# Performance work log

Hardware: AMD Instinct MI355X
Metric: run time of the kernel (lower is better)

## Reference

```python
import jax, jax.numpy as jnp
import numpy as np

B, D_MODEL, H, W = 4, 128, 128, 128
HEAD_DIM = 16
GROUP = D_MODEL // HEAD_DIM          # 8 deformable groups
D_INNER = D_MODEL                    # expand = 1
D_STATE = 1
DT_RANK = 8                          # ceil(d_model / 16)
D_CONV = 3
EPS = 1e-6


def setup_inputs() -> dict:
    key = jax.random.key(0)
    ks = jax.random.split(key, 10)
    f = jnp.float32
    # dt bias init as in DASSM.dt_init (dt in [1e-3, 1e-1], inverse-softplus)
    dt = jnp.exp(jax.random.uniform(ks[7], (D_INNER,), f)
                 * (np.log(0.1) - np.log(0.001)) + np.log(0.001))
    dt = jnp.clip(dt, 1e-4)
    dt_b = dt + jnp.log(-jnp.expm1(-dt))
    s = DT_RANK ** -0.5
    return dict(
        x=jax.random.normal(ks[0], (B, D_MODEL, H, W), f),
        in_proj_w=jax.random.normal(ks[1], (D_INNER, D_MODEL), f) * (D_MODEL ** -0.5),
        conv2d_w=jax.random.normal(ks[2], (D_INNER, 1, D_CONV, D_CONV), f) * 0.1,
        conv2d_b=jnp.zeros((D_INNER,), f),
        dw_w=jax.random.normal(ks[3], (D_INNER, 1, 3, 3), f) * 0.1,
        dw_b=jnp.zeros((D_INNER,), f),
        dw_ln_g=jnp.ones((D_INNER,), f),
        dw_ln_b=jnp.zeros((D_INNER,), f),
        off_w=jax.random.normal(ks[4], (GROUP * 2, D_INNER), f) * 0.01,
        off_b=jnp.zeros((GROUP * 2,), f),
        x_proj_w=jax.random.normal(ks[5], (DT_RANK + 2 * D_STATE, D_INNER), f) * (D_INNER ** -0.5),
        dt_w=jax.random.uniform(ks[6], (D_INNER, DT_RANK), f, -s, s),
        dt_b=dt_b,
        A_logs=jnp.tile(jnp.log(jnp.arange(1, D_STATE + 1, dtype=f))[None, :], (D_INNER, 1)),
        Ds=jnp.ones((D_INNER,), f),
        out_ln_g=jnp.ones((D_INNER,), f),
        out_ln_b=jnp.zeros((D_INNER,), f),
        out_proj_w=jax.random.normal(ks[8], (D_MODEL, D_INNER), f) * (D_INNER ** -0.5),
    )


def _layer_norm(x, g, b):
    m = x.mean(-1, keepdims=True)
    v = ((x - m) ** 2).mean(-1, keepdims=True)
    return (x - m) * jax.lax.rsqrt(v + EPS) * g + b


def _dwconv(x, w, b):
    # x: (B,C,H,W), w: (C,1,k,k) depthwise, 'SAME' == torch padding=(k-1)//2
    out = jax.lax.conv_general_dilated(
        x, w, (1, 1), 'SAME', feature_group_count=x.shape[1],
        dimension_numbers=('NCHW', 'OIHW', 'NCHW'))
    return out + b[None, :, None, None]


def _dcn_sample(img_last, offset):
    # DCNv3 with kernel_size=1, mask=1: sampling point = pixel center + offset.
    # img_last: (B,H,W,C); offset: (B,H,W,G*2) laid out (x,y) per group.
    b, h, w, c = img_last.shape
    gc = c // GROUP
    img = img_last.reshape(b, h, w, GROUP, gc)
    off = offset.reshape(b, h, w, GROUP, 2)
    px = jnp.arange(w, dtype=offset.dtype)[None, None, :, None] + off[..., 0]
    py = jnp.arange(h, dtype=offset.dtype)[None, :, None, None] + off[..., 1]
    y0 = jnp.floor(py)
    x0 = jnp.floor(px)
    wy = py - y0
    wx = px - x0
    bi = jnp.arange(b)[:, None, None, None]
    gi = jnp.arange(GROUP)[None, None, None, :]

    def tap(yi, xi, wgt):  # zero-padding bilinear tap (grid_sample, align_corners=False)
        valid = (yi >= 0) & (yi < h) & (xi >= 0) & (xi < w)
        yc = jnp.clip(yi, 0, h - 1).astype(jnp.int32)
        xc = jnp.clip(xi, 0, w - 1).astype(jnp.int32)
        v = img[bi, yc, xc, gi]  # (B,H,W,G,gc)
        return v * (wgt * valid)[..., None]

    out = (tap(y0, x0, (1 - wy) * (1 - wx)) + tap(y0, x0 + 1, (1 - wy) * wx)
           + tap(y0 + 1, x0, wy * (1 - wx)) + tap(y0 + 1, x0 + 1, wy * wx))
    return out.reshape(b, h, w, c)


def _selective_scan(xs, dts, A, Bs, Cs, Ds, dt_bias):
    # xs,dts: (B,D,L); A: (D,N); Bs,Cs: (B,N,L); delta_softplus=True
    delta = jax.nn.softplus(dts + dt_bias[None, :, None])
    dA = jnp.exp(jnp.einsum('bdl,dn->lbdn', delta, A))          # (L,B,D,N)
    dBx = jnp.einsum('bdl,bnl,bdl->lbdn', delta, Bs, xs)          # (L,B,D,N)
    C_t = jnp.transpose(Cs, (2, 0, 1))                            # (L,B,N)

    def step(hc, inputs):
        dA_t, dBx_t, c = inputs
        hc = dA_t * hc + dBx_t
        return hc, jnp.einsum('bdn,bn->bd', hc, c)

    h0 = jnp.zeros(dA.shape[1:], xs.dtype)
    _, ys = jax.lax.scan(step, h0, (dA, dBx, C_t))                # ys: (L,B,D)
    y = jnp.transpose(ys, (1, 2, 0))                              # (B,D,L)
    return y + Ds[None, :, None] * xs


def reference(x, in_proj_w, conv2d_w, conv2d_b, dw_w, dw_b, dw_ln_g, dw_ln_b,
              off_w, off_b, x_proj_w, dt_w, dt_b, A_logs, Ds,
              out_ln_g, out_ln_b, out_proj_w):
    # in_proj (1x1 conv, no bias) then depthwise conv + SiLU
    xin = jnp.einsum('bchw,oc->bohw', x, in_proj_w)
    xc = jax.nn.silu(_dwconv(xin, conv2d_w, conv2d_b))
    # Dynamic_Adaptive_Scan: dwconv -> LN(channels_last) -> GELU -> offsets -> DCNv3(k=1)
    x1 = _dwconv(xc, dw_w, dw_b)
    x1 = jax.nn.gelu(_layer_norm(jnp.transpose(x1, (0, 2, 3, 1)), dw_ln_g, dw_ln_b),
                     approximate=False)
    offset = x1 @ off_w.T + off_b                                  # (B,H,W,G*2)
    xd = _dcn_sample(jnp.transpose(xc, (0, 2, 3, 1)), offset)      # (B,H,W,C)
    xd = jnp.transpose(xd, (0, 3, 1, 2))                           # (B,C,H,W)
    # SSM (Mamba selective scan over L = H*W)
    Bn, C, Hh, Ww = xd.shape
    L = Hh * Ww
    xs = xd.reshape(Bn, C, L)
    x_dbl = jnp.einsum('rc,bcl->brl', x_proj_w, xs)
    dts, Bs, Cs = jnp.split(x_dbl, [DT_RANK, DT_RANK + D_STATE], axis=1)
    dts = jnp.einsum('dr,brl->bdl', dt_w, dts)
    A = -jnp.exp(A_logs)
    y = _selective_scan(xs, dts, A, Bs, Cs, Ds, dt_b).reshape(Bn, C, Hh, Ww)
    # out LayerNorm (over channels) + out_proj (1x1, no bias)
    y = jnp.transpose(_layer_norm(jnp.transpose(y, (0, 2, 3, 1)), out_ln_g, out_ln_b),
                      (0, 3, 1, 2))
    return jnp.einsum('bchw,oc->bohw', y, out_proj_w)
```

## Files before the change

### kernel.cpp

```cpp
#include <hip/hip_runtime.h>
#include <hip/hip_bf16.h>

typedef unsigned short u16;
typedef unsigned int u32;
typedef __bf16 bf16x8 __attribute__((ext_vector_type(8)));
typedef float f32x4 __attribute__((ext_vector_type(4)));

__device__ __forceinline__ float bfu(u16 u) { return __uint_as_float(((u32)u) << 16); }
__device__ __forceinline__ u16 fbf(float f) {
  __hip_bfloat16 h = __float2bfloat16(f);
  return *reinterpret_cast<u16*>(&h);
}
__device__ __forceinline__ float softplusf(float z) {
  float t = __expf(z);
  return (z > 20.f) ? z : __logf(1.f + t);
}
__device__ __forceinline__ float lo16(u32 p) { return __uint_as_float(p << 16); }
__device__ __forceinline__ float hi16(u32 p) { return __uint_as_float(p & 0xffff0000u); }
__device__ __forceinline__ bf16x8 ld_bf8(const u16* p) {
  union { uint4 u; bf16x8 v; } c;
  c.u = *(const uint4*)p;
  return c.v;
}


__global__ __launch_bounds__(256) void k_inproj(const float* __restrict__ X,
                                                const float* __restrict__ W,
                                                u16* __restrict__ out,
                                                const float* __restrict__ W2,
                                                const float* __restrict__ gO,
                                                const float* __restrict__ bO,
                                                float* __restrict__ s12) {
  __shared__ __align__(16) u16 Ws[128 * 136];
  __shared__ __align__(16) u16 Xs[64 * 136];
  int tid = threadIdx.x;
  if (blockIdx.x == 1024) {
    if (tid < 128) {
      int o = tid;
      float s1 = 0.f, s2 = 0.f;
      for (int c = 0; c < 128; ++c) {
        float w = W2[(o << 7) + c];
        s1 = fmaf(w, bO[c], s1);
        s2 = fmaf(w, gO[c], s2);
      }
      s12[o] = s1;
      s12[128 + o] = s2;
    }
    return;
  }
  int b = blockIdx.x >> 8;
  int l0 = (blockIdx.x & 255) << 6;
  for (int i = 0; i < 16; ++i) {
    int idx = (i << 8) + tid;
    int o = idx >> 5, c4 = (idx & 31) << 2;
    float4 w4 = *(const float4*)&W[(o << 7) + c4];
    ushort4 s;
    s.x = fbf(w4.x); s.y = fbf(w4.y); s.z = fbf(w4.z); s.w = fbf(w4.w);
    *(ushort4*)&Ws[o * 136 + c4] = s;
  }
  for (int i = 0; i < 8; ++i) {
    int idx = (i << 8) + tid;
    int c = idx >> 4, lq = (idx & 15) << 2;
    float4 x4 = *(const float4*)&X[(((long)(b << 7) + c) << 14) + l0 + lq];
    Xs[(lq + 0) * 136 + c] = fbf(x4.x);
    Xs[(lq + 1) * 136 + c] = fbf(x4.y);
    Xs[(lq + 2) * 136 + c] = fbf(x4.z);
    Xs[(lq + 3) * 136 + c] = fbf(x4.w);
  }
  __syncthreads();
  int w = tid >> 6, lane = tid & 63;
  int mrow = lane & 15, quad = lane >> 4;
  f32x4 acc[2][4];
#pragma unroll
  for (int ot = 0; ot < 2; ++ot)
#pragma unroll
    for (int lt = 0; lt < 4; ++lt) acc[ot][lt] = (f32x4){0.f, 0.f, 0.f, 0.f};
#pragma unroll
  for (int kb = 0; kb < 4; ++kb) {
    int c0 = (kb << 5) + (quad << 3);
    bf16x8 af[2], bfr[4];
#pragma unroll
    for (int ot = 0; ot < 2; ++ot)
      af[ot] = ld_bf8(&Ws[((w << 5) + (ot << 4) + mrow) * 136 + c0]);
#pragma unroll
    for (int lt = 0; lt < 4; ++lt)
      bfr[lt] = ld_bf8(&Xs[((lt << 4) + mrow) * 136 + c0]);
#pragma unroll
    for (int ot = 0; ot < 2; ++ot)
#pragma unroll
      for (int lt = 0; lt < 4; ++lt)
        acc[ot][lt] = __builtin_amdgcn_mfma_f32_16x16x32_bf16(af[ot], bfr[lt], acc[ot][lt], 0, 0, 0);
  }
#pragma unroll
  for (int ot = 0; ot < 2; ++ot)
#pragma unroll
    for (int lt = 0; lt < 4; ++lt) {
      int l = l0 + (lt << 4) + mrow;
      int o = (w << 5) + (ot << 4) + (quad << 2);
      ushort4 s;
      s.x = fbf(acc[ot][lt][0]); s.y = fbf(acc[ot][lt][1]);
      s.z = fbf(acc[ot][lt][2]); s.w = fbf(acc[ot][lt][3]);
      *(ushort4*)&out[(((long)(b << 14) + l) << 7) + o] = s;
    }
}

__global__ __launch_bounds__(256) void k_dwconv(const u16* __restrict__ in,
                                                const float* __restrict__ w9,
                                                const float* __restrict__ bias,
                                                u16* __restrict__ out) {
  __shared__ float wsT[9][128];
  __shared__ float bs[128];
  int tid = threadIdx.x;
  for (int i = 0; i < 5; ++i) {
    int lin = (i << 8) + tid;
    if (lin < 1152) { int c = lin / 9, k = lin - 9 * c; wsT[k][c] = w9[lin]; }
  }
  if (tid < 128) bs[tid] = bias[tid];
  __syncthreads();
  int blk = blockIdx.x;
  int b = blk >> 10;
  int s = blk & 1023;
  int h = s >> 3;
  int w = ((s & 7) << 4) + (tid >> 4);
  int c0 = (tid & 15) << 3;
  const u16* bbase = in + ((long)b << 21);
  float acc[8];
  {
    float4 b0 = *(const float4*)&bs[c0];
    float4 b1 = *(const float4*)&bs[c0 + 4];
    acc[0] = b0.x; acc[1] = b0.y; acc[2] = b0.z; acc[3] = b0.w;
    acc[4] = b1.x; acc[5] = b1.y; acc[6] = b1.z; acc[7] = b1.w;
  }
#pragma unroll
  for (int ky = -1; ky <= 1; ++ky) {
    int y = h + ky;
    if ((unsigned)y >= 128u) continue;
#pragma unroll
    for (int kx = -1; kx <= 1; ++kx) {
      int x = w + kx;
      if ((unsigned)x >= 128u) continue;
      int k = (ky + 1) * 3 + (kx + 1);
      uint4 v = *(const uint4*)(bbase + ((((y << 7) + x)) << 7) + c0);
      float4 w0 = *(const float4*)&wsT[k][c0];
      float4 w1 = *(const float4*)&wsT[k][c0 + 4];
      u32 vv[4] = {v.x, v.y, v.z, v.w};
      float wf[8] = {w0.x, w0.y, w0.z, w0.w, w1.x, w1.y, w1.z, w1.w};
#pragma unroll
      for (int cc = 0; cc < 8; ++cc) {
        float xv = (cc & 1) ? hi16(vv[cc >> 1]) : lo16(vv[cc >> 1]);
        acc[cc] = fmaf(wf[cc], xv, acc[cc]);
      }
    }
  }
#pragma unroll
  for (int cc = 0; cc < 8; ++cc) acc[cc] = acc[cc] / (1.f + __expf(-acc[cc]));
  int g4 = c0 >> 4, sub = c0 & 15;
  uint4 pkst;
  pkst.x = (u32)fbf(acc[0]) | ((u32)fbf(acc[1]) << 16);
  pkst.y = (u32)fbf(acc[2]) | ((u32)fbf(acc[3]) << 16);
  pkst.z = (u32)fbf(acc[4]) | ((u32)fbf(acc[5]) << 16);
  pkst.w = (u32)fbf(acc[6]) | ((u32)fbf(acc[7]) << 16);
  u16* po = out + (((long)(b << 3) + g4) << 18) + ((((h << 7) + w)) << 4) + sub;
  *(uint4*)po = pkst;
}

__global__ __launch_bounds__(256) void k_dwoff(const u16* __restrict__ in,
                                               const float* __restrict__ w9,
                                               const float* __restrict__ bias,
                                               const float* __restrict__ g,
                                               const float* __restrict__ bt,
                                               const float* __restrict__ offw,
                                               const float* __restrict__ offb,
                                               float* __restrict__ offs) {
  __shared__ float wsT[9][128];
  __shared__ float bs[128], gs[128], bsh[128];
  __shared__ __align__(16) u16 Ge[16 * 136];
  __shared__ __align__(16) u16 Wos[16 * 136];
  int tid = threadIdx.x;
  for (int i = 0; i < 5; ++i) {
    int lin = (i << 8) + tid;
    if (lin < 1152) { int c = lin / 9, k = lin - 9 * c; wsT[k][c] = w9[lin]; }
  }
  if (tid < 128) { bs[tid] = bias[tid]; gs[tid] = g[tid]; bsh[tid] = bt[tid]; }
  for (int i = 0; i < 8; ++i) {
    int idx = (i << 8) + tid;
    int o = idx >> 7, c = idx & 127;
    Wos[o * 136 + c] = fbf(offw[idx]);
  }
  __syncthreads();
  int blk = blockIdx.x;
  int b = blk >> 10;
  int s = blk & 1023;
  int h = s >> 3;
  int p = tid >> 4;
  int w = ((s & 7) << 4) + p;
  int c0 = (tid & 15) << 3;
  int g4 = c0 >> 4, sub = c0 & 15;
  const u16* bbase = in + (((long)(b << 3) + g4) << 18) + sub;
  float acc[8];
  {
    float4 b0 = *(const float4*)&bs[c0];
    float4 b1 = *(const float4*)&bs[c0 + 4];
    acc[0] = b0.x; acc[1] = b0.y; acc[2] = b0.z; acc[3] = b0.w;
    acc[4] = b1.x; acc[5] = b1.y; acc[6] = b1.z; acc[7] = b1.w;
  }
#pragma unroll
  for (int ky = -1; ky <= 1; ++ky) {
    int y = h + ky;
    if ((unsigned)y >= 128u) continue;
#pragma unroll
    for (int kx = -1; kx <= 1; ++kx) {
      int x = w + kx;
      if ((unsigned)x >= 128u) continue;
      int k = (ky + 1) * 3 + (kx + 1);
      uint4 v = *(const uint4*)(bbase + ((((y << 7) + x)) << 4));
      float4 w0 = *(const float4*)&wsT[k][c0];
      float4 w1 = *(const float4*)&wsT[k][c0 + 4];
      u32 vv[4] = {v.x, v.y, v.z, v.w};
      float wf[8] = {w0.x, w0.y, w0.z, w0.w, w1.x, w1.y, w1.z, w1.w};
#pragma unroll
      for (int cc = 0; cc < 8; ++cc) {
        float xv = (cc & 1) ? hi16(vv[cc >> 1]) : lo16(vv[cc >> 1]);
        acc[cc] = fmaf(wf[cc], xv, acc[cc]);
      }
    }
  }
  float sum = 0.f, ssum = 0.f;
#pragma unroll
  for (int cc = 0; cc < 8; ++cc) { sum += acc[cc]; ssum = fmaf(acc[cc], acc[cc], ssum); }
#pragma unroll
  for (int off = 1; off < 16; off <<= 1) {
    sum += __shfl_xor(sum, off);
    ssum += __shfl_xor(ssum, off);
  }
  float m = sum * (1.f / 128.f);
  float r = rsqrtf(ssum * (1.f / 128.f) - m * m + 1e-6f);
  {
    u32 pk[4];
#pragma unroll
    for (int jj = 0; jj < 4; ++jj) {
      u16 h2[2];
#pragma unroll
      for (int e = 0; e < 2; ++e) {
        int cc = 2 * jj + e;
        float xn = fmaf((acc[cc] - m) * r, gs[c0 + cc], bsh[c0 + cc]);
        h2[e] = fbf(0.5f * xn * (1.f + erff(xn * 0.70710678118f)));
      }
      pk[jj] = (u32)h2[0] | ((u32)h2[1] << 16);
    }
    *(uint4*)&Ge[p * 136 + c0] = make_uint4(pk[0], pk[1], pk[2], pk[3]);
  }
  __syncthreads();
  if (tid < 64) {
    int lane = tid;
    int mrow = lane & 15, quad = lane >> 4;
    f32x4 acc0 = (f32x4){0.f, 0.f, 0.f, 0.f};
#pragma unroll
    for (int kb = 0; kb < 4; ++kb) {
      int cb = (kb << 5) + (quad << 3);
      bf16x8 af = ld_bf8(&Wos[mrow * 136 + cb]);
      bf16x8 bfr = ld_bf8(&Ge[mrow * 136 + cb]);
      acc0 = __builtin_amdgcn_mfma_f32_16x16x32_bf16(af, bfr, acc0, 0, 0, 0);
    }
    int l = (h << 7) + ((s & 7) << 4) + mrow;
    float2* po = (float2*)offs;
    int o0 = quad << 2;
    po[(((long)((b << 3) + (quad << 1))) << 14) + l] =
        make_float2(acc0[0] + offb[o0], acc0[1] + offb[o0 + 1]);
    po[(((long)((b << 3) + (quad << 1) + 1)) << 14) + l] =
        make_float2(acc0[2] + offb[o0 + 2], acc0[3] + offb[o0 + 3]);
  }
}

__global__ __launch_bounds__(512, 8) void k_dcn(const u16* __restrict__ xc,
                                                const float* __restrict__ offs,
                                                const float* __restrict__ xpw,
                                                const float* __restrict__ dtw,
                                                u16* __restrict__ xs,
                                                u16* __restrict__ dts,
                                                float* __restrict__ Bsb,
                                                float* __restrict__ Csb) {
  __shared__ __align__(16) u16 xds_bf[64 * 132];
  __shared__ float part[64 * 81];
  __shared__ __align__(16) float xdblT[8 * 64];
  int tid = threadIdx.x;
  int blk = blockIdx.x;
  int b = blk >> 8;
  int l0 = (blk & 255) << 6;
  int p = tid & 63, gg = tid >> 6;
  int l = l0 + p, hh = l >> 7, ww = l & 127;
  float2 off = ((const float2*)offs)[(((long)((b << 3) + gg)) << 14) + l];
  float px = (float)ww + off.x, py = (float)hh + off.y;
  float x0f = floorf(px), y0f = floorf(py);
  float wx = px - x0f, wy = py - y0f;
  int ix = (int)x0f, iy = (int)y0f;
  int x0c = min(max(ix, 0), 127), x1c = min(max(ix + 1, 0), 127);
  int y0c = min(max(iy, 0), 127), y1c = min(max(iy + 1, 0), 127);
  float vx0 = ((unsigned)ix < 128u) ? 1.f : 0.f;
  float vx1 = ((unsigned)(ix + 1) < 128u) ? 1.f : 0.f;
  float vy0 = ((unsigned)iy < 128u) ? 1.f : 0.f;
  float vy1 = ((unsigned)(iy + 1) < 128u) ? 1.f : 0.f;
  float wt4[4] = {(1.f - wy) * (1.f - wx) * vy0 * vx0,
                  (1.f - wy) * wx * vy0 * vx1,
                  wy * (1.f - wx) * vy1 * vx0,
                  wy * wx * vy1 * vx1};
  const u16* bbase = xc + (((long)(b << 3) + gg) << 18);
  const u16* r0p = bbase + ((((y0c << 7) + x0c)) << 4);
  const u16* r1p = bbase + ((((y1c << 7) + x0c)) << 4);
  uint4 q0 = ((const uint4*)r0p)[0];
  uint4 q1 = ((const uint4*)r0p)[1];
  uint4 q2 = ((const uint4*)r0p)[2];
  uint4 q3 = ((const uint4*)r0p)[3];
  uint4 q4 = ((const uint4*)r1p)[0];
  uint4 q5 = ((const uint4*)r1p)[1];
  uint4 q6 = ((const uint4*)r1p)[2];
  uint4 q7 = ((const uint4*)r1p)[3];
  bool adj = (x1c != x0c);
  u32 t0[8] = {q0.x, q0.y, q0.z, q0.w, q1.x, q1.y, q1.z, q1.w};
  u32 t1[8] = {adj ? q2.x : q0.x, adj ? q2.y : q0.y, adj ? q2.z : q0.z, adj ? q2.w : q0.w,
               adj ? q3.x : q1.x, adj ? q3.y : q1.y, adj ? q3.z : q1.z, adj ? q3.w : q1.w};
  u32 t2[8] = {q4.x, q4.y, q4.z, q4.w, q5.x, q5.y, q5.z, q5.w};
  u32 t3[8] = {adj ? q6.x : q4.x, adj ? q6.y : q4.y, adj ? q6.z : q4.z, adj ? q6.w : q4.w,
               adj ? q7.x : q5.x, adj ? q7.y : q5.y, adj ? q7.z : q5.z, adj ? q7.w : q5.w};
  float acc[16];
#pragma unroll
  for (int ch = 0; ch < 16; ++ch) acc[ch] = 0.f;
#pragma unroll
  for (int ch = 0; ch < 16; ++ch) {
    float v0 = (ch & 1) ? hi16(t0[ch >> 1]) : lo16(t0[ch >> 1]);
    float v1 = (ch & 1) ? hi16(t1[ch >> 1]) : lo16(t1[ch >> 1]);
    float v2 = (ch & 1) ? hi16(t2[ch >> 1]) : lo16(t2[ch >> 1]);
    float v3 = (ch & 1) ? hi16(t3[ch >> 1]) : lo16(t3[ch >> 1]);
    float a = fmaf(wt4[0], v0, wt4[1] * v1);
    a = fmaf(wt4[2], v2, a);
    acc[ch] = fmaf(wt4[3], v3, a);
  }
  {
    u32 pk[8];
#pragma unroll
    for (int j = 0; j < 8; ++j)
      pk[j] = (u32)fbf(acc[2 * j]) | ((u32)fbf(acc[2 * j + 1]) << 16);
    u16* row = &xds_bf[p * 132 + (gg << 4)];
#pragma unroll
    for (int q = 0; q < 4; ++q)
      *(uint2*)(row + (q << 2)) = make_uint2(pk[2 * q], pk[2 * q + 1]);
  }
  {
    int ggu = __builtin_amdgcn_readfirstlane(gg);
    const float* wb = xpw + (ggu << 4);
    int pbase = p * 81 + gg;
#pragma unroll
    for (int r = 0; r < 10; ++r) {
      const float* wr = wb + (r << 7);
      float s = 0.f;
#pragma unroll
      for (int ch = 0; ch < 16; ++ch) s = fmaf(wr[ch], acc[ch], s);
      part[pbase + (r << 3)] = s;
    }
  }
  __syncthreads();
  {
    int task = tid;
#pragma unroll
    for (int pass = 0; pass < 2; ++pass, task += 512) {
      if (task < 640) {
        int r = task >> 6, p2 = task & 63;
        const float* pp = &part[p2 * 81 + (r << 3)];
        float s = ((pp[0] + pp[1]) + (pp[2] + pp[3])) + ((pp[4] + pp[5]) + (pp[6] + pp[7]));
        if (r < 8) xdblT[(r << 6) + p2] = s;
        else if (r == 8) Bsb[((long)b << 14) + l0 + p2] = s;
        else Csb[((long)b << 14) + l0 + p2] = s;
      }
    }
  }
#pragma unroll
  for (int it = 0; it < 2; ++it) {
    int task = (it << 9) + tid;
    int cc = task >> 3, t = task & 7;
    u32 pk[4];
#pragma unroll
    for (int jj = 0; jj < 4; ++jj) {
      u16 a0 = xds_bf[((t << 3) + 2 * jj + 0) * 132 + cc];
      u16 a1 = xds_bf[((t << 3) + 2 * jj + 1) * 132 + cc];
      pk[jj] = (u32)a0 | ((u32)a1 << 16);
    }
    *(uint4*)&xs[(((long)(b << 7) + cc) << 14) + l0 + (t << 3)] =
        make_uint4(pk[0], pk[1], pk[2], pk[3]);
  }
  __syncthreads();
  {
    int dd = tid >> 3, t = tid & 7;
    float4 a0 = *(const float4*)&dtw[dd << 3];
    float4 a1 = *(const float4*)&dtw[(dd << 3) + 4];
    float4 b0 = *(const float4*)&dtw[(dd + 64) << 3];
    float4 b1 = *(const float4*)&dtw[((dd + 64) << 3) + 4];
    float wr0[8] = {a0.x, a0.y, a0.z, a0.w, a1.x, a1.y, a1.z, a1.w};
    float wr1[8] = {b0.x, b0.y, b0.z, b0.w, b1.x, b1.y, b1.z, b1.w};
    float y0[8], y1[8];
#pragma unroll
    for (int j = 0; j < 8; ++j) { y0[j] = 0.f; y1[j] = 0.f; }
#pragma unroll
    for (int rr = 0; rr < 8; ++rr) {
      float w0 = wr0[rr], w1 = wr1[rr];
      const float* xr = &xdblT[(rr << 6) + (t << 3)];
      float4 xa = *(const float4*)xr;
      float4 xb = *(const float4*)(xr + 4);
      float xv[8] = {xa.x, xa.y, xa.z, xa.w, xb.x, xb.y, xb.z, xb.w};
#pragma unroll
      for (int j = 0; j < 8; ++j) {
        y0[j] = fmaf(w0, xv[j], y0[j]);
        y1[j] = fmaf(w1, xv[j], y1[j]);
      }
    }
    u32 pk0[4], pk1[4];
#pragma unroll
    for (int jj = 0; jj < 4; ++jj) {
      pk0[jj] = (u32)fbf(y0[2 * jj]) | ((u32)fbf(y0[2 * jj + 1]) << 16);
      pk1[jj] = (u32)fbf(y1[2 * jj]) | ((u32)fbf(y1[2 * jj + 1]) << 16);
    }
    *(uint4*)&dts[(((long)(b << 7) + dd) << 14) + l0 + (t << 3)] =
        make_uint4(pk0[0], pk0[1], pk0[2], pk0[3]);
    *(uint4*)&dts[(((long)(b << 7) + dd + 64) << 14) + l0 + (t << 3)] =
        make_uint4(pk1[0], pk1[1], pk1[2], pk1[3]);
  }
}

__global__ __launch_bounds__(1024) void k_scan(u16* __restrict__ xy,
                                               const u16* __restrict__ dts16,
                                               const float* __restrict__ Bsb,
                                               const float* __restrict__ Csb,
                                               const float* __restrict__ A_logs,
                                               const float* __restrict__ Dsv,
                                               const float* __restrict__ dtbv) {
  __shared__ float swp[16], swe[16];
  int bd = blockIdx.x;
  int b = bd >> 7, d = bd & 127;
  float Ad = -__expf(A_logs[d]);
  float dtb = dtbv[d];
  float Dd = Dsv[d];
  int t = threadIdx.x;
  int lane = t & 63, wid = t >> 6;
  long base = ((long)bd << 14) + (t << 4);
  long bb = ((long)b << 14) + (t << 4);
  const uint4* pz4 = (const uint4*)(dts16 + base);
  const uint4* px4 = (const uint4*)(xy + base);
  const float4* pB = (const float4*)(Bsb + bb);
  const float4* pC = (const float4*)(Csb + bb);
  uint4 zA = pz4[0], zB = pz4[1];
  uint4 xA = px4[0], xB = px4[1];
  u32 zw[8] = {zA.x, zA.y, zA.z, zA.w, zB.x, zB.y, zB.z, zB.w};
  u32 xw[8] = {xA.x, xA.y, xA.z, xA.w, xB.x, xB.y, xB.z, xB.w};
  float E = 0.f, P = 1.f;
#pragma unroll
  for (int q = 0; q < 4; ++q) {
    float4 B4 = pB[q];
    float Bq[4] = {B4.x, B4.y, B4.z, B4.w};
#pragma unroll
    for (int j = 0; j < 4; ++j) {
      int k = (q << 2) + j;
      float z = (k & 1) ? hi16(zw[k >> 1]) : lo16(zw[k >> 1]);
      float xv = (k & 1) ? hi16(xw[k >> 1]) : lo16(xw[k >> 1]);
      float delta = softplusf(z + dtb);
      float a = __expf(delta * Ad);
      E = fmaf(a, E, delta * Bq[j] * xv);
      P *= a;
    }
  }
#pragma unroll
  for (int off = 1; off < 64; off <<= 1) {
    float Pp = __shfl_up(P, off);
    float Ep = __shfl_up(E, off);
    if (lane >= off) { E = fmaf(P, Ep, E); P *= Pp; }
  }
  if (lane == 63) { swp[wid] = P; swe[wid] = E; }
  __syncthreads();
  if (t < 16) {
    float p2 = swp[t], e2 = swe[t];
#pragma unroll
    for (int off = 1; off < 16; off <<= 1) {
      float pp = __shfl_up(p2, off);
      float ee = __shfl_up(e2, off);
      if (t >= off) { e2 = fmaf(p2, ee, e2); p2 *= pp; }
    }
    swp[t] = p2; swe[t] = e2;
  }
  __syncthreads();
  float hw = (wid == 0) ? 0.f : swe[wid - 1];
  float Pex = __shfl_up(P, 1);
  float Eex = __shfl_up(E, 1);
  if (lane == 0) { Pex = 1.f; Eex = 0.f; }
  float h = fmaf(Pex, hw, Eex);
  u32 ypk[8];
#pragma unroll
  for (int q = 0; q < 4; ++q) {
    float4 B4 = pB[q];
    float4 C4 = pC[q];
    float Bq[4] = {B4.x, B4.y, B4.z, B4.w};
    float Cq[4] = {C4.x, C4.y, C4.z, C4.w};
#pragma unroll
    for (int j = 0; j < 4; ++j) {
      int k = (q << 2) + j;
      float z = (k & 1) ? hi16(zw[k >> 1]) : lo16(zw[k >> 1]);
      float xv = (k & 1) ? hi16(xw[k >> 1]) : lo16(xw[k >> 1]);
      float delta = softplusf(z + dtb);
      float a = __expf(delta * Ad);
      h = fmaf(a, h, delta * Bq[j] * xv);
      u16 yb = fbf(fmaf(Dd, xv, h * Cq[j]));
      if ((k & 1) == 0) ypk[k >> 1] = yb; else ypk[k >> 1] |= (u32)yb << 16;
    }
  }
  uint4* py = (uint4*)(xy + base);
  py[0] = make_uint4(ypk[0], ypk[1], ypk[2], ypk[3]);
  py[1] = make_uint4(ypk[4], ypk[5], ypk[6], ypk[7]);
}

__global__ __launch_bounds__(256) void k_outproj(const u16* __restrict__ y,
                                                 const float* __restrict__ W2,
                                                 const float* __restrict__ g,
                                                 const float* __restrict__ s12,
                                                 float* __restrict__ out) {
  __shared__ __align__(16) u16 Ws[128 * 136];
  __shared__ __align__(16) u16 Ys[64 * 136];
  __shared__ float ps[4][64], pss[4][64];
  __shared__ float mean_s[64], rstd_s[64];
  int tid = threadIdx.x;
  int b = blockIdx.x >> 8;
  int l0 = (blockIdx.x & 255) << 6;
  for (int i = 0; i < 16; ++i) {
    int idx = (i << 8) + tid;
    int o = idx >> 5, c4 = (idx & 31) << 2;
    float4 w4 = *(const float4*)&W2[(o << 7) + c4];
    ushort4 s;
    s.x = fbf(w4.x * g[c4]);     s.y = fbf(w4.y * g[c4 + 1]);
    s.z = fbf(w4.z * g[c4 + 2]); s.w = fbf(w4.w * g[c4 + 3]);
    *(ushort4*)&Ws[o * 136 + c4] = s;
  }
  for (int i = 0; i < 4; ++i) {
    int idx = (i << 8) + tid;
    int c = idx >> 3, lq = (idx & 7) << 3;
    uint4 v = *(const uint4*)&y[(((long)(b << 7) + c) << 14) + l0 + lq];
    u32 vv[4] = {v.x, v.y, v.z, v.w};
#pragma unroll
    for (int r = 0; r < 8; ++r)
      Ys[(lq + r) * 136 + c] = (u16)((r & 1) ? (vv[r >> 1] >> 16) : (vv[r >> 1] & 0xffffu));
  }
  __syncthreads();
  {
    int l = tid & 63, q = tid >> 6;
    const u16* row = &Ys[l * 136 + (q << 5)];
    float s = 0.f, ss = 0.f;
#pragma unroll 8
    for (int c = 0; c < 32; ++c) { float v = bfu(row[c]); s += v; ss = fmaf(v, v, ss); }
    ps[q][l] = s; pss[q][l] = ss;
  }
  __syncthreads();
  if (tid < 64) {
    float s = ps[0][tid] + ps[1][tid] + ps[2][tid] + ps[3][tid];
    float ss = pss[0][tid] + pss[1][tid] + pss[2][tid] + pss[3][tid];
    float m = s * (1.f / 128.f);
    mean_s[tid] = m;
    rstd_s[tid] = rsqrtf(ss * (1.f / 128.f) - m * m + 1e-6f);
  }
  __syncthreads();
  int w = tid >> 6, lane = tid & 63;
  int mrow = lane & 15, quad = lane >> 4;
  f32x4 acc[2][4];
#pragma unroll
  for (int ot = 0; ot < 2; ++ot)
#pragma unroll
    for (int lt = 0; lt < 4; ++lt) acc[ot][lt] = (f32x4){0.f, 0.f, 0.f, 0.f};
#pragma unroll
  for (int kb = 0; kb < 4; ++kb) {
    int c0 = (kb << 5) + (quad << 3);
    bf16x8 af[2], bfr[4];
#pragma unroll
    for (int ot = 0; ot < 2; ++ot)
      af[ot] = ld_bf8(&Ws[((w << 5) + (ot << 4) + mrow) * 136 + c0]);
#pragma unroll
    for (int lt = 0; lt < 4; ++lt)
      bfr[lt] = ld_bf8(&Ys[((lt << 4) + mrow) * 136 + c0]);
#pragma unroll
    for (int ot = 0; ot < 2; ++ot)
#pragma unroll
      for (int lt = 0; lt < 4; ++lt)
        acc[ot][lt] = __builtin_amdgcn_mfma_f32_16x16x32_bf16(af[ot], bfr[lt], acc[ot][lt], 0, 0, 0);
  }
  float s1r[2][4], s2r[2][4];
#pragma unroll
  for (int ot = 0; ot < 2; ++ot)
#pragma unroll
    for (int r = 0; r < 4; ++r) {
      int o = (w << 5) + (ot << 4) + (quad << 2) + r;
      s1r[ot][r] = s12[o];
      s2r[ot][r] = s12[128 + o];
    }
#pragma unroll
  for (int ot = 0; ot < 2; ++ot)
#pragma unroll
    for (int lt = 0; lt < 4; ++lt) {
      int lcol = (lt << 4) + mrow;
      float mv = mean_s[lcol], rv = rstd_s[lcol];
      int obase = (w << 5) + (ot << 4) + (quad << 2);
#pragma unroll
      for (int r = 0; r < 4; ++r) {
        float v = fmaf(rv, acc[ot][lt][r] - mv * s2r[ot][r], s1r[ot][r]);
        out[(((long)(b << 7) + obase + r) << 14) + l0 + lcol] = v;
      }
    }
}

extern "C" void kernel_launch(void* const* d_in, const int* in_sizes, int n_in,
                              void* d_out, int out_size, void* d_ws, size_t ws_size,
                              hipStream_t stream) {
  const float* x         = (const float*)d_in[0];
  const float* in_proj_w = (const float*)d_in[1];
  const float* conv2d_w  = (const float*)d_in[2];
  const float* conv2d_b  = (const float*)d_in[3];
  const float* dw_w      = (const float*)d_in[4];
  const float* dw_b      = (const float*)d_in[5];
  const float* dw_ln_g   = (const float*)d_in[6];
  const float* dw_ln_b   = (const float*)d_in[7];
  const float* off_w     = (const float*)d_in[8];
  const float* off_b     = (const float*)d_in[9];
  const float* x_proj_w  = (const float*)d_in[10];
  const float* dt_w      = (const float*)d_in[11];
  const float* dt_b      = (const float*)d_in[12];
  const float* A_logs    = (const float*)d_in[13];
  const float* Ds        = (const float*)d_in[14];
  const float* out_ln_g  = (const float*)d_in[15];
  const float* out_ln_b  = (const float*)d_in[16];
  const float* out_proj_w= (const float*)d_in[17];
  float* out = (float*)d_out;

  u16* A  = (u16*)d_ws;
  u16* Bx = A + 8388608;
  u16* Dd = Bx + 8388608;
  float* offs  = (float*)(Dd + 8388608);
  float* Bsb   = offs + 1048576;
  float* Csb   = Bsb + 65536;
  float* s12   = Csb + 65536;

  hipLaunchKernelGGL(k_inproj, dim3(1025), dim3(256), 0, stream, x, in_proj_w, A,
                     out_proj_w, out_ln_g, out_ln_b, s12);
  hipLaunchKernelGGL(k_dwconv, dim3(4096), dim3(256), 0, stream, A, conv2d_w, conv2d_b, Bx);
  hipLaunchKernelGGL(k_dwoff, dim3(4096), dim3(256), 0, stream, Bx, dw_w, dw_b,
                     dw_ln_g, dw_ln_b, off_w, off_b, offs);
  hipLaunchKernelGGL(k_dcn, dim3(1024), dim3(512), 0, stream, Bx, offs, x_proj_w, dt_w, A, Dd, Bsb, Csb);
  hipLaunchKernelGGL(k_scan, dim3(512), dim3(1024), 0, stream, A, Dd, Bsb, Csb, A_logs, Ds, dt_b);
  hipLaunchKernelGGL(k_outproj, dim3(1024), dim3(256), 0, stream, A, out_proj_w, out_ln_g, s12, out);
}
```

Measured before the change: 218.8 us.

## Fuse offset-generation kernel into deformable sampling kernel via shared memory

Merges the depthwise conv + LayerNorm + GELU + offset-projection kernel into the DCN sampling kernel, so each 64-pixel block computes its own offsets into shared memory instead of writing them to global memory and reading them back. This removes one launch and the global round-trip of the offset buffer. Shared memory is aliased across phases through a union buffer, and launch bounds drop from 8 to 6 blocks per SM. Each thread now handles 16 channels of the dwconv with per-element weight loads from LDS, which may raise register pressure and lower occupancy.

Measured after the change: 209.5 us. 4.3% less time.

```diff
diff --git a/kernel.cpp b/kernel.cpp
--- a/kernel.cpp
+++ b/kernel.cpp
@@ -164,132 +164,120 @@
   *(uint4*)po = pkst;
 }
 
-__global__ __launch_bounds__(256) void k_dwoff(const u16* __restrict__ in,
-                                               const float* __restrict__ w9,
-                                               const float* __restrict__ bias,
-                                               const float* __restrict__ g,
-                                               const float* __restrict__ bt,
-                                               const float* __restrict__ offw,
-                                               const float* __restrict__ offb,
-                                               float* __restrict__ offs) {
-  __shared__ float wsT[9][128];
+__global__ __launch_bounds__(512, 6) void k_dcnoff(const u16* __restrict__ xc,
+                                                   const float* __restrict__ w9,
+                                                   const float* __restrict__ bias,
+                                                   const float* __restrict__ g,
+                                                   const float* __restrict__ bt,
+                                                   const float* __restrict__ offw,
+                                                   const float* __restrict__ offb,
+                                                   const float* __restrict__ xpw,
+                                                   const float* __restrict__ dtw,
+                                                   u16* __restrict__ xs,
+                                                   u16* __restrict__ dts,
+                                                   float* __restrict__ Bsb,
+                                                   float* __restrict__ Csb) {
+  __shared__ __align__(16) char uni[26368];
   __shared__ float bs[128], gs[128], bsh[128];
-  __shared__ __align__(16) u16 Ge[16 * 136];
-  __shared__ __align__(16) u16 Wos[16 * 136];
+  __shared__ __align__(16) u16 xds_bf[64 * 132];
+  __shared__ __align__(16) float xdblT[8 * 64];
+  __shared__ __align__(16) float2 offsL[64 * 8];
+  u16* Ge = (u16*)uni;
+  float* wsT2 = (float*)(uni + 17408);
+  u16* Wos = (u16*)(uni + 22016);
+  float* part = (float*)uni;
   int tid = threadIdx.x;
-  for (int i = 0; i < 5; ++i) {
-    int lin = (i << 8) + tid;
-    if (lin < 1152) { int c = lin / 9, k = lin - 9 * c; wsT[k][c] = w9[lin]; }
+  for (int i = 0; i < 3; ++i) {
+    int lin = (i << 9) + tid;
+    if (lin < 1152) wsT2[lin] = w9[lin];
   }
   if (tid < 128) { bs[tid] = bias[tid]; gs[tid] = g[tid]; bsh[tid] = bt[tid]; }
-  for (int i = 0; i < 8; ++i) {
-    int idx = (i << 8) + tid;
+  for (int i = 0; i < 4; ++i) {
+    int idx = (i << 9) + tid;
     int o = idx >> 7, c = idx & 127;
     Wos[o * 136 + c] = fbf(offw[idx]);
   }
-  __syncthreads();
-  int blk = blockIdx.x;
-  int b = blk >> 10;
-  int s = blk & 1023;
-  int h = s >> 3;
-  int p = tid >> 4;
-  int w = ((s & 7) << 4) + p;
-  int c0 = (tid & 15) << 3;
-  int g4 = c0 >> 4, sub = c0 & 15;
-  const u16* bbase = in + (((long)(b << 3) + g4) << 18) + sub;
-  float acc[8];
-  {
-    float4 b0 = *(const float4*)&bs[c0];
-    float4 b1 = *(const float4*)&bs[c0 + 4];
-    acc[0] = b0.x; acc[1] = b0.y; acc[2] = b0.z; acc[3] = b0.w;
-    acc[4] = b1.x; acc[5] = b1.y; acc[6] = b1.z; acc[7] = b1.w;
-  }
-#pragma unroll
-  for (int ky = -1; ky <= 1; ++ky) {
-    int y = h + ky;
-    if ((unsigned)y >= 128u) continue;
-#pragma unroll
-    for (int kx = -1; kx <= 1; ++kx) {
-      int x = w + kx;
-      if ((unsigned)x >= 128u) continue;
-      int k = (ky + 1) * 3 + (kx + 1);
-      uint4 v = *(const uint4*)(bbase + ((((y << 7) + x)) << 4));
-      float4 w0 = *(const float4*)&wsT[k][c0];
-      float4 w1 = *(const float4*)&wsT[k][c0 + 4];
-      u32 vv[4] = {v.x, v.y, v.z, v.w};
-      float wf[8] = {w0.x, w0.y, w0.z, w0.w, w1.x, w1.y, w1.z, w1.w};
-#pragma unroll
-      for (int cc = 0; cc < 8; ++cc) {
-        float xv = (cc & 1) ? hi16(vv[cc >> 1]) : lo16(vv[cc >> 1]);
-        acc[cc] = fmaf(wf[cc], xv, acc[cc]);
-      }
-    }
-  }
-  float sum = 0.f, ssum = 0.f;
-#pragma unroll
-  for (int cc = 0; cc < 8; ++cc) { sum += acc[cc]; ssum = fmaf(acc[cc], acc[cc], ssum); }
-#pragma unroll
-  for (int off = 1; off < 16; off <<= 1) {
-    sum += __shfl_xor(sum, off);
-    ssum += __shfl_xor(ssum, off);
-  }
-  float m = sum * (1.f / 128.f);
-  float r = rsqrtf(ssum * (1.f / 128.f) - m * m + 1e-6f);
-  {
-    u32 pk[4];
-#pragma unroll
-    for (int jj = 0; jj < 4; ++jj) {
-      u16 h2[2];
-#pragma unroll
-      for (int e = 0; e < 2; ++e) {
-        int cc = 2 * jj + e;
-        float xn = fmaf((acc[cc] - m) * r, gs[c0 + cc], bsh[c0 + cc]);
-        h2[e] = fbf(0.5f * xn * (1.f + erff(xn * 0.70710678118f)));
-      }
-      pk[jj] = (u32)h2[0] | ((u32)h2[1] << 16);
-    }
-    *(uint4*)&Ge[p * 136 + c0] = make_uint4(pk[0], pk[1], pk[2], pk[3]);
-  }
-  __syncthreads();
-  if (tid < 64) {
-    int lane = tid;
-    int mrow = lane & 15, quad = lane >> 4;
-    f32x4 acc0 = (f32x4){0.f, 0.f, 0.f, 0.f};
-#pragma unroll
-    for (int kb = 0; kb < 4; ++kb) {
-      int cb = (kb << 5) + (quad << 3);
-      bf16x8 af = ld_bf8(&Wos[mrow * 136 + cb]);
-      bf16x8 bfr = ld_bf8(&Ge[mrow * 136 + cb]);
-      acc0 = __builtin_amdgcn_mfma_f32_16x16x32_bf16(af, bfr, acc0, 0, 0, 0);
-    }
-    int l = (h << 7) + ((s & 7) << 4) + mrow;
-    float2* po = (float2*)offs;
-    int o0 = quad << 2;
-    po[(((long)((b << 3) + (quad << 1))) << 14) + l] =
-        make_float2(acc0[0] + offb[o0], acc0[1] + offb[o0 + 1]);
-    po[(((long)((b << 3) + (quad << 1) + 1)) << 14) + l] =
-        make_float2(acc0[2] + offb[o0 + 2], acc0[3] + offb[o0 + 3]);
-  }
-}
-
-__global__ __launch_bounds__(512, 8) void k_dcn(const u16* __restrict__ xc,
-                                                const float* __restrict__ offs,
-                                                const float* __restrict__ xpw,
-                                                const float* __restrict__ dtw,
-                                                u16* __restrict__ xs,
-                                                u16* __restrict__ dts,
-                                                float* __restrict__ Bsb,
-                                                float* __restrict__ Csb) {
-  __shared__ __align__(16) u16 xds_bf[64 * 132];
-  __shared__ float part[64 * 81];
-  __shared__ __align__(16) float xdblT[8 * 64];
-  int tid = threadIdx.x;
   int blk = blockIdx.x;
   int b = blk >> 8;
   int l0 = (blk & 255) << 6;
+  __syncthreads();
+  {
+    int p2 = tid >> 3, g2 = tid & 7;
+    int l = l0 + p2, hh = l >> 7, ww = l & 127;
+    const u16* bb2 = xc + (((long)(b << 3) + g2) << 18);
+    float acc[16];
+#pragma unroll
+    for (int cc = 0; cc < 16; ++cc) acc[cc] = bs[(g2 << 4) + cc];
+#pragma unroll
+    for (int ky = -1; ky <= 1; ++ky) {
+      int y = hh + ky;
+      if ((unsigned)y >= 128u) continue;
+#pragma unroll
+      for (int kx = -1; kx <= 1; ++kx) {
+        int x = ww + kx;
+        if ((unsigned)x >= 128u) continue;
+        int k = (ky + 1) * 3 + (kx + 1);
+        const u16* tp = bb2 + ((((y << 7) + x)) << 4);
+        uint4 v0 = *(const uint4*)tp;
+        uint4 v1 = *(const uint4*)(tp + 8);
+        u32 vv[8] = {v0.x, v0.y, v0.z, v0.w, v1.x, v1.y, v1.z, v1.w};
+#pragma unroll
+        for (int cc = 0; cc < 16; ++cc) {
+          float wv = wsT2[((g2 << 4) + cc) * 9 + k];
+          float xv = (cc & 1) ? hi16(vv[cc >> 1]) : lo16(vv[cc >> 1]);
+          acc[cc] = fmaf(wv, xv, acc[cc]);
+        }
+      }
+    }
+    float sum = 0.f, ssum = 0.f;
+#pragma unroll
+    for (int cc = 0; cc < 16; ++cc) { sum += acc[cc]; ssum = fmaf(acc[cc], acc[cc], ssum); }
+#pragma unroll
+    for (int off = 1; off < 8; off <<= 1) {
+      sum += __shfl_xor(sum, off);
+      ssum += __shfl_xor(ssum, off);
+    }
+    float m = sum * (1.f / 128.f);
+    float r = rsqrtf(ssum * (1.f / 128.f) - m * m + 1e-6f);
+    u32 pk[8];
+#pragma unroll
+    for (int jj = 0; jj < 8; ++jj) {
+      u16 h2[2];
+#pragma unroll
+      for (int e = 0; e < 2; ++e) {
+        int cc = 2 * jj + e;
+        float xn = fmaf((acc[cc] - m) * r, gs[(g2 << 4) + cc], bsh[(g2 << 4) + cc]);
+        h2[e] = fbf(0.5f * xn * (1.f + erff(xn * 0.70710678118f)));
+      }
+      pk[jj] = (u32)h2[0] | ((u32)h2[1] << 16);
+    }
+    u16* row = &Ge[p2 * 136 + (g2 << 4)];
+    *(uint4*)row = make_uint4(pk[0], pk[1], pk[2], pk[3]);
+    *(uint4*)(row + 8) = make_uint4(pk[4], pk[5], pk[6], pk[7]);
+  }
+  __syncthreads();
+  {
+    int w = tid >> 6, lane = tid & 63;
+    if (w < 4) {
+      int mrow = lane & 15, quad = lane >> 4;
+      f32x4 acc0 = (f32x4){0.f, 0.f, 0.f, 0.f};
+#pragma unroll
+      for (int kb = 0; kb < 4; ++kb) {
+        int cb = (kb << 5) + (quad << 3);
+        bf16x8 af = ld_bf8(&Wos[mrow * 136 + cb]);
+        bf16x8 bfr = ld_bf8(&Ge[((w << 4) + mrow) * 136 + cb]);
+        acc0 = __builtin_amdgcn_mfma_f32_16x16x32_bf16(af, bfr, acc0, 0, 0, 0);
+      }
+      int p = (w << 4) + mrow;
+      int o0 = quad << 2;
+      offsL[(p << 3) + (quad << 1)] = make_float2(acc0[0] + offb[o0], acc0[1] + offb[o0 + 1]);
+      offsL[(p << 3) + (quad << 1) + 1] = make_float2(acc0[2] + offb[o0 + 2], acc0[3] + offb[o0 + 3]);
+    }
+  }
+  __syncthreads();
   int p = tid & 63, gg = tid >> 6;
   int l = l0 + p, hh = l >> 7, ww = l & 127;
-  float2 off = ((const float2*)offs)[(((long)((b << 3) + gg)) << 14) + l];
+  float2 off = offsL[(p << 3) + gg];
   float px = (float)ww + off.x, py = (float)hh + off.y;
   float x0f = floorf(px), y0f = floorf(py);
   float wx = px - x0f, wy = py - y0f;
@@ -324,8 +312,6 @@
                adj ? q7.x : q5.x, adj ? q7.y : q5.y, adj ? q7.z : q5.z, adj ? q7.w : q5.w};
   float acc[16];
 #pragma unroll
-  for (int ch = 0; ch < 16; ++ch) acc[ch] = 0.f;
-#pragma unroll
   for (int ch = 0; ch < 16; ++ch) {
     float v0 = (ch & 1) ? hi16(t0[ch >> 1]) : lo16(t0[ch >> 1]);
     float v1 = (ch & 1) ? hi16(t1[ch >> 1]) : lo16(t1[ch >> 1]);
@@ -635,17 +621,15 @@
   u16* A  = (u16*)d_ws;
   u16* Bx = A + 8388608;
   u16* Dd = Bx + 8388608;
-  float* offs  = (float*)(Dd + 8388608);
-  float* Bsb   = offs + 1048576;
+  float* Bsb   = (float*)(Dd + 8388608);
   float* Csb   = Bsb + 65536;
   float* s12   = Csb + 65536;
 
   hipLaunchKernelGGL(k_inproj, dim3(1025), dim3(256), 0, stream, x, in_proj_w, A,
                      out_proj_w, out_ln_g, out_ln_b, s12);
   hipLaunchKernelGGL(k_dwconv, dim3(4096), dim3(256), 0, stream, A, conv2d_w, conv2d_b, Bx);
-  hipLaunchKernelGGL(k_dwoff, dim3(4096), dim3(256), 0, stream, Bx, dw_w, dw_b,
-                     dw_ln_g, dw_ln_b, off_w, off_b, offs);
-  hipLaunchKernelGGL(k_dcn, dim3(1024), dim3(512), 0, stream, Bx, offs, x_proj_w, dt_w, A, Dd, Bsb, Csb);
+  hipLaunchKernelGGL(k_dcnoff, dim3(1024), dim3(512), 0, stream, Bx, dw_w, dw_b,
+                     dw_ln_g, dw_ln_b, off_w, off_b, x_proj_w, dt_w, A, Dd, Bsb, Csb);
   hipLaunchKernelGGL(k_scan, dim3(512), dim3(1024), 0, stream, A, Dd, Bsb, Csb, A_logs, Ds, dt_b);
   hipLaunchKernelGGL(k_outproj, dim3(1024), dim3(256), 0, stream, A, out_proj_w, out_ln_g, s12, out);
 }
```
